# Performance work log

Hardware: AMD Instinct MI355X
Metric: run time of the kernel (lower is better)

The kernel has to match this reference:

```python
import jax, jax.numpy as jnp
import numpy as np

HEADS = 8
TOK = 4  # num_query_tokens
EPS = 1e-5


def _ln(x, w, b):
    mu = jnp.mean(x, -1, keepdims=True)
    v = jnp.var(x, -1, keepdims=True)
    return (x - mu) / jnp.sqrt(v + EPS) * w + b


def _inorm(x):
    # InstanceNorm3d(affine=False): normalize per (B,C) over spatial dims
    mu = jnp.mean(x, (2, 3, 4), keepdims=True)
    v = jnp.var(x, (2, 3, 4), keepdims=True)
    return (x - mu) / jnp.sqrt(v + EPS)


def _conv3(x, w, b):
    y = jax.lax.conv_general_dilated(x, w, (1, 1, 1), 'SAME',
                                     dimension_numbers=('NCDHW', 'OIDHW', 'NCDHW'))
    return y + b[None, :, None, None, None]


def setup_inputs() -> dict:
    key = jax.random.key(0)
    ks = jax.random.split(key, 8)
    B, C, D, H, W = 4, 320, 16, 32, 32
    CLI = 320
    QD = C * TOK  # 1280
    s = 0.02
    return {
        'img_feat': jax.random.normal(ks[0], (B, C, D, H, W), jnp.float32),
        'cli_feat': jax.random.normal(ks[1], (B, CLI), jnp.float32),
        'Wq': jax.random.normal(ks[2], (QD, CLI), jnp.float32) * s,
        'bq': jnp.zeros((QD,), jnp.float32),
        'lnq_w': jnp.ones((QD,), jnp.float32),
        'lnq_b': jnp.zeros((QD,), jnp.float32),
        'Wk': jax.random.normal(ks[3], (C, C), jnp.float32) * s,
        'bk': jnp.zeros((C,), jnp.float32),
        'Wv': jax.random.normal(ks[4], (C, C), jnp.float32) * s,
        'bv': jnp.zeros((C,), jnp.float32),
        'Wo': jax.random.normal(ks[5], (C, QD), jnp.float32) * s,
        'bo': jnp.zeros((C,), jnp.float32),
        'lno_w': jnp.ones((C,), jnp.float32),
        'lno_b': jnp.zeros((C,), jnp.float32),
        'Wf1': jax.random.normal(ks[6], (C, 2 * C, 3, 3, 3), jnp.float32) * s,
        'bf1': jnp.zeros((C,), jnp.float32),
        'Wf2': jax.random.normal(ks[7], (C, C, 3, 3, 3), jnp.float32) * s,
        'bf2': jnp.zeros((C,), jnp.float32),
    }


def reference(img_feat, cli_feat, Wq, bq, lnq_w, lnq_b, Wk, bk, Wv, bv,
              Wo, bo, lno_w, lno_b, Wf1, bf1, Wf2, bf2):
    B, C, D, H, W = img_feat.shape
    S = D * H * W
    hd = C // HEADS
    scale = hd ** -0.5
    # clinical features -> 4 query tokens per head: [B, heads, head_dim, TOK]
    q = _ln(cli_feat @ Wq.T + bq, lnq_w, lnq_b).reshape(B, HEADS, hd, TOK)
    # 1x1x1 convs == per-position linear over channels
    x = img_feat.reshape(B, C, S)
    k = (jnp.einsum('oc,bcs->bos', Wk, x) + bk[None, :, None]).reshape(B, HEADS, hd, S)
    v = (jnp.einsum('oc,bcs->bos', Wv, x) + bv[None, :, None]).reshape(B, HEADS, hd, S)
    # [B, heads, TOK, S] scores -> softmax over spatial
    attn = jax.nn.softmax(jnp.einsum('bhdt,bhds->bhts', q, k) * scale, axis=-1)
    # value @ attn^T -> [B, heads, head_dim, TOK], flatten like torch .view(B,-1)
    o = jnp.einsum('bhds,bhts->bhdt', v, attn).reshape(B, HEADS * hd * TOK)
    o = _ln(o @ Wo.T + bo, lno_w, lno_b)  # [B, C]
    bcast = jnp.broadcast_to(o[:, :, None, None, None], (B, C, D, H, W))
    fused = jnp.concatenate([img_feat, bcast], axis=1)  # [B, 2C, D, H, W]
    h = jax.nn.gelu(_inorm(_conv3(fused, Wf1, bf1)), approximate=False)
    h = _inorm(_conv3(h, Wf2, bf2))
    return h + img_feat
```

## Files before the change

kernel.cpp:

```cpp
#include <hip/hip_runtime.h>
#include <hip/hip_bf16.h>
#include <math.h>

typedef unsigned short u16;

#define DEV static __device__ __forceinline__

DEV float bfu(u16 u) { union { unsigned int i; float f; } v; v.i = ((unsigned int)u) << 16; return v.f; }
DEV u16 fbu(float f) { __hip_bfloat16 h = __float2bfloat16(f); return *reinterpret_cast<u16*>(&h); }

template <typename T> struct ModeOf;
template <> struct ModeOf<u16>   { static constexpr int v = 0; };
template <> struct ModeOf<float> { static constexpr int v = 1; };
template <typename T> DEV float ld(const void* p, size_t i);
template <> DEV float ld<u16>(const void* p, size_t i)   { return bfu(((const u16*)p)[i]); }
template <> DEV float ld<float>(const void* p, size_t i) { return ((const float*)p)[i]; }

DEV float dot8f(const float* img, size_t idx, const float* ar, int s) {
    const float4 x0 = *reinterpret_cast<const float4*>(img + idx + s);
    const float4 x1 = *reinterpret_cast<const float4*>(img + idx + s + 4);
    const float4 a0 = *reinterpret_cast<const float4*>(ar + s);
    const float4 a1 = *reinterpret_cast<const float4*>(ar + s + 4);
    return a0.x*x0.x + a0.y*x0.y + a0.z*x0.z + a0.w*x0.w
         + a1.x*x1.x + a1.y*x1.y + a1.z*x1.z + a1.w*x1.w;
}

#define NB 4
#define NC 320
#define ND 16
#define NH 32
#define NW 32
#define NS 16384
#define NHD 40
#define NQD 1280
#define NR 32
#define NTOK 4
#define OUT_N (NB*NC*NS)
#define EPSV 1e-5f
#define SCALE 0.15811388300841898f

#define YKS 8
#define YCH (NS / YKS)
#define YKC 32
#define YCS (NS / YKC)

#define CSL 32
#define NSL 10
#define HALO_D 4
#define HALO_H 6
#define PIXW 34
#define NPIX (HALO_D*HALO_H*PIXW)
#define PACKN (27*10*20*64*8)

typedef __attribute__((ext_vector_type(8))) short bf16x8;
typedef __attribute__((ext_vector_type(4))) float f32x4;

DEV int swz4(int p) { return (p + (p >> 2)) & 3; }

DEV float blk_sum(float v, float* red) {
    __syncthreads();
#pragma unroll
    for (int o = 32; o > 0; o >>= 1) v += __shfl_down(v, o, 64);
    int wv = threadIdx.x >> 6, ln = threadIdx.x & 63;
    if (ln == 0) red[wv] = v;
    __syncthreads();
    return red[0] + red[1] + red[2] + red[3];
}
DEV float blk_max(float v, float* red) {
    __syncthreads();
#pragma unroll
    for (int o = 32; o > 0; o >>= 1) v = fmaxf(v, __shfl_down(v, o, 64));
    int wv = threadIdx.x >> 6, ln = threadIdx.x & 63;
    if (ln == 0) red[wv] = v;
    __syncthreads();
    return fmaxf(fmaxf(red[0], red[1]), fmaxf(red[2], red[3]));
}

__global__ void detect_kernel(const u16* __restrict__ lnqw, int* __restrict__ flag) {
    if (threadIdx.x == 0) flag[0] = (lnqw[0] == 0x3F80) ? 0 : 1;
}

template <typename T>
__global__ __launch_bounds__(256) void q_kernel(const int* __restrict__ flag,
        const void* __restrict__ cli, const void* __restrict__ Wq, const void* __restrict__ bq,
        const void* __restrict__ lnw, const void* __restrict__ lnb, float* __restrict__ qout) {
    if (*flag != ModeOf<T>::v) return;
    int b = blockIdx.x, tid = threadIdx.x;
    __shared__ float cl[NC];
    __shared__ float red[8];
    for (int i = tid; i < NC; i += 256) cl[i] = ld<T>(cli, b * NC + i);
    __syncthreads();
    float loc[5];
    float s1 = 0.f, s2 = 0.f;
#pragma unroll
    for (int k = 0; k < 5; ++k) {
        int j = tid + k * 256;
        float a = ld<T>(bq, j);
        size_t wr = (size_t)j * NC;
        for (int c = 0; c < NC; ++c) a += cl[c] * ld<T>(Wq, wr + c);
        loc[k] = a; s1 += a; s2 += a * a;
    }
    s1 = blk_sum(s1, red);
    s2 = blk_sum(s2, red);
    float mu = s1 / (float)NQD;
    float var = fmaxf(s2 / (float)NQD - mu * mu, 0.f);
    float rs = rsqrtf(var + EPSV);
#pragma unroll
    for (int k = 0; k < 5; ++k) {
        int j = tid + k * 256;
        qout[(size_t)b * NQD + j] = (loc[k] - mu) * rs * ld<T>(lnw, j) + ld<T>(lnb, j);
    }
}

template <typename T>
__global__ __launch_bounds__(256) void qw_kernel(const int* __restrict__ flag,
        const float* __restrict__ q, const void* __restrict__ Wk, const void* __restrict__ bk,
        float* __restrict__ qW, float* __restrict__ qb, u16* __restrict__ qwb) {
    if (*flag != ModeOf<T>::v) return;
    int gid = blockIdx.x * 256 + threadIdx.x;
    if (gid < NB * NR * NC) {
        int c = gid % NC;
        int r = (gid / NC) % NR;
        int b = gid / (NC * NR);
        int h = r >> 2, t = r & 3;
        float a = 0.f;
        const float* qb_ = q + (size_t)b * NQD;
        for (int d = 0; d < NHD; ++d)
            a += qb_[(h * NHD + d) * NTOK + t] * ld<T>(Wk, (size_t)(h * NHD + d) * NC + c);
        qW[gid] = a;
        int kk = c >> 5, gg = (c >> 3) & 3, j = c & 7;
        int mf = r >> 4, lane = (gg << 4) | (r & 15);
        qwb[(((size_t)(b * 10 + kk) * 2 + mf) << 9) + (lane << 3) + j] = fbu(a);
    }
    if (gid < NB * NR) {
        int r = gid & 31, b = gid >> 5;
        int h = r >> 2, t = r & 3;
        float a = 0.f;
        const float* qb_ = q + (size_t)b * NQD;
        for (int d = 0; d < NHD; ++d)
            a += qb_[(h * NHD + d) * NTOK + t] * ld<T>(bk, h * NHD + d);
        qb[gid] = a;
    }
}

__global__ __launch_bounds__(256) void scores_mm_kernel(
        const u16* __restrict__ imgt, const u16* __restrict__ qwb,
        const float* __restrict__ qb, float* __restrict__ attn) {
    int b = blockIdx.y;
    int s0 = blockIdx.x * 256 + (threadIdx.x >> 6) * 64;
    int ln = threadIdx.x & 63;
    int col = ln & 15, g = ln >> 4;
    bf16x8 af[10][2];
    const u16* qa = qwb + (size_t)b * 10 * 2 * 512;
#pragma unroll
    for (int kk = 0; kk < 10; ++kk)
#pragma unroll
        for (int mf = 0; mf < 2; ++mf)
            af[kk][mf] = *reinterpret_cast<const bf16x8*>(qa + (((kk << 1) + mf) << 9) + (ln << 3));
    f32x4 acc[2][4];
#pragma unroll
    for (int mf = 0; mf < 2; ++mf)
#pragma unroll
        for (int nf = 0; nf < 4; ++nf) acc[mf][nf] = (f32x4){0.f, 0.f, 0.f, 0.f};
    const u16* xb = imgt + (size_t)b * NS * NC;
#pragma unroll
    for (int kk = 0; kk < 10; ++kk) {
#pragma unroll
        for (int nf = 0; nf < 4; ++nf) {
            bf16x8 bf = *reinterpret_cast<const bf16x8*>(
                xb + (size_t)(s0 + nf * 16 + col) * NC + kk * 32 + (g << 3));
#pragma unroll
            for (int mf = 0; mf < 2; ++mf)
                acc[mf][nf] = __builtin_amdgcn_mfma_f32_16x16x32_bf16(
                    af[kk][mf], bf, acc[mf][nf], 0, 0, 0);
        }
    }
#pragma unroll
    for (int mf = 0; mf < 2; ++mf)
#pragma unroll
        for (int nf = 0; nf < 4; ++nf)
#pragma unroll
            for (int r = 0; r < 4; ++r) {
                int row = mf * 16 + g * 4 + r;
                attn[((size_t)(b * NR + row) << 14) + s0 + nf * 16 + col] =
                    (acc[mf][nf][r] + qb[b * NR + row]) * SCALE;
            }
}

__global__ __launch_bounds__(256) void smax_part_kernel(const float* __restrict__ attn,
        float* __restrict__ pm, float* __restrict__ pl) {
    int row = blockIdx.x, kc = blockIdx.y;
    const float* rp = attn + ((size_t)row << 14) + kc * 2048;
    __shared__ float red[8];
    int t4 = threadIdx.x * 4;
    float4 v0 = *reinterpret_cast<const float4*>(rp + t4);
    float4 v1 = *reinterpret_cast<const float4*>(rp + t4 + 1024);
    float m = fmaxf(fmaxf(fmaxf(v0.x, v0.y), fmaxf(v0.z, v0.w)),
                    fmaxf(fmaxf(v1.x, v1.y), fmaxf(v1.z, v1.w)));
    m = blk_max(m, red);
    float s = expf(v0.x - m) + expf(v0.y - m) + expf(v0.z - m) + expf(v0.w - m)
            + expf(v1.x - m) + expf(v1.y - m) + expf(v1.z - m) + expf(v1.w - m);
    s = blk_sum(s, red);
    if (threadIdx.x == 0) { pm[row * 8 + kc] = m; pl[row * 8 + kc] = s; }
}

__global__ __launch_bounds__(128) void smax_comb_kernel(const float* __restrict__ pm,
        const float* __restrict__ pl, float* __restrict__ gm, float* __restrict__ gli) {
    int row = threadIdx.x;
    float M = -1e30f;
#pragma unroll
    for (int k = 0; k < 8; ++k) M = fmaxf(M, pm[row * 8 + k]);
    float L = 0.f;
#pragma unroll
    for (int k = 0; k < 8; ++k) L += pl[row * 8 + k] * expf(pm[row * 8 + k] - M);
    gm[row] = M; gli[row] = 1.f / L;
}

__global__ __launch_bounds__(256) void smax_fin_kernel(float* __restrict__ attn,
        const float* __restrict__ gm, const float* __restrict__ gli, u16* __restrict__ attnb) {
    int row = blockIdx.x, kc = blockIdx.y;
    size_t base = ((size_t)row << 14) + kc * 2048;
    float M = gm[row], LI = gli[row];
    int t4 = threadIdx.x * 4;
#pragma unroll
    for (int h = 0; h < 2; ++h) {
        size_t i = base + t4 + h * 1024;
        float4 v = *reinterpret_cast<const float4*>(attn + i);
        v.x = expf(v.x - M) * LI; v.y = expf(v.y - M) * LI;
        v.z = expf(v.z - M) * LI; v.w = expf(v.w - M) * LI;
        *reinterpret_cast<float4*>(attn + i) = v;
        ushort4 bv; bv.x = fbu(v.x); bv.y = fbu(v.y); bv.z = fbu(v.z); bv.w = fbu(v.w);
        *reinterpret_cast<ushort4*>(attnb + i) = bv;
    }
}

__global__ __launch_bounds__(256) void ymm_kernel(const int* __restrict__ flag,
        const u16* __restrict__ attnb, const void* __restrict__ img, float* __restrict__ yp) {
    if (*flag != 0) return;
    int kc = blockIdx.x, ct = blockIdx.y, b = blockIdx.z;
    int wv = threadIdx.x >> 6, ln = threadIdx.x & 63;
    int col = ln & 15, g = ln >> 4;
    int s0 = kc * YCS;
    const u16* imgB = (const u16*)img;
    const u16* ap0 = attnb + (((size_t)b * 32 + col) << 14) + s0 + (g << 3);
    const u16* bp  = imgB + (((size_t)(b * NC + ct * 64 + wv * 16 + col)) << 14) + s0 + (g << 3);
    f32x4 acc[2];
    acc[0] = (f32x4){0.f, 0.f, 0.f, 0.f};
    acc[1] = (f32x4){0.f, 0.f, 0.f, 0.f};
#pragma unroll
    for (int ks = 0; ks < YCS / 32; ++ks) {
        bf16x8 bf = *reinterpret_cast<const bf16x8*>(bp + ks * 32);
        bf16x8 a0 = *reinterpret_cast<const bf16x8*>(ap0 + ks * 32);
        bf16x8 a1 = *reinterpret_cast<const bf16x8*>(ap0 + (16 << 14) + ks * 32);
        acc[0] = __builtin_amdgcn_mfma_f32_16x16x32_bf16(a0, bf, acc[0], 0, 0, 0);
        acc[1] = __builtin_amdgcn_mfma_f32_16x16x32_bf16(a1, bf, acc[1], 0, 0, 0);
    }
    int c = ct * 64 + wv * 16 + col;
#pragma unroll
    for (int mf = 0; mf < 2; ++mf)
#pragma unroll
        for (int r = 0; r < 4; ++r) {
            int row = b * 32 + mf * 16 + g * 4 + r;
            yp[((size_t)kc * NB * NR + row) * NC + c] = acc[mf][r];
        }
}

template <typename T>
__global__ __launch_bounds__(256) void y_kernel(const int* __restrict__ flag,
        const float* __restrict__ attn, const void* __restrict__ img, float* __restrict__ yp) {
    if (*flag != ModeOf<T>::v) return;
    int row = blockIdx.x;
    int ks  = blockIdx.y;
    int b = row >> 5;
    int wv = threadIdx.x >> 6, ln = threadIdx.x & 63;
    const float* ar = attn + ((size_t)row << 14) + ks * YCH;
    size_t xb = (size_t)b * NC * NS + ks * YCH;
    float* yout = yp + ((size_t)ks * NB * NR + row) * NC;
    for (int c = wv; c < NC; c += 4) {
        size_t xr = xb + ((size_t)c << 14);
        float p = 0.f;
#pragma unroll
        for (int it = 0; it < YCH / 512; ++it)
            p += dot8f((const float*)img, xr, ar, it * 512 + ln * 8);
#pragma unroll
        for (int o = 32; o > 0; o >>= 1) p += __shfl_down(p, o, 64);
        if (ln == 0) yout[c] = p;
    }
}

__global__ __launch_bounds__(256) void yred_kernel(const int* __restrict__ flag, int mode, int nk,
        const float* __restrict__ yp, float* __restrict__ y) {
    if (*flag != mode) return;
    int i = blockIdx.x * 256 + threadIdx.x;
    if (i >= NB * NR * NC) return;
    float s = 0.f;
    for (int k = 0; k < nk; ++k) s += yp[(size_t)k * NB * NR * NC + i];
    y[i] = s;
}

template <typename T>
__global__ __launch_bounds__(256) void o_kernel(const int* __restrict__ flag,
        const float* __restrict__ y, const void* __restrict__ Wv, const void* __restrict__ bv,
        const void* __restrict__ Wo, const void* __restrict__ bo,
        const void* __restrict__ lnw, const void* __restrict__ lnb, float* __restrict__ o2) {
    if (*flag != ModeOf<T>::v) return;
    int b = blockIdx.x, tid = threadIdx.x;
    __shared__ float yl[NR * NC];
    __shared__ float ol[NQD];
    __shared__ float red[8];
    for (int i = tid; i < NR * NC; i += 256) yl[i] = y[(size_t)b * NR * NC + i];
    __syncthreads();
#pragma unroll
    for (int k = 0; k < 5; ++k) {
        int i = tid + k * 256;
        int h = i / 160, rem = i - h * 160;
        int d = rem >> 2, t = rem & 3;
        int wr = h * NHD + d, r = h * NTOK + t;
        float a = ld<T>(bv, wr);
        size_t wvr = (size_t)wr * NC;
        const float* yr = yl + r * NC;
        for (int c = 0; c < NC; ++c) a += ld<T>(Wv, wvr + c) * yr[c];
        ol[i] = a;
    }
    __syncthreads();
    for (int j = tid; j < NC; j += 256) {
        float a = ld<T>(bo, j);
        size_t wor = (size_t)j * NQD;
        for (int i = 0; i < NQD; ++i) a += ld<T>(Wo, wor + i) * ol[i];
        yl[j] = a;
    }
    __syncthreads();
    float s1 = 0.f, s2 = 0.f;
    for (int j = tid; j < NC; j += 256) { float v = yl[j]; s1 += v; s2 += v * v; }
    s1 = blk_sum(s1, red);
    s2 = blk_sum(s2, red);
    float mu = s1 / (float)NC;
    float var = fmaxf(s2 / (float)NC - mu * mu, 0.f);
    float rs = rsqrtf(var + EPSV);
    for (int j = tid; j < NC; j += 256)
        o2[(size_t)b * NC + j] = (yl[j] - mu) * rs * ld<T>(lnw, j) + ld<T>(lnb, j);
}

template <typename T>
__global__ __launch_bounds__(256) void p_kernel(const int* __restrict__ flag,
        const float* __restrict__ o2, const void* __restrict__ Wf1, float* __restrict__ P) {
    if (*flag != ModeOf<T>::v) return;
    int o = blockIdx.x, b = blockIdx.y;
    int tid = threadIdx.x, wv = tid >> 6, ln = tid & 63;
    __shared__ float red[4 * 27];
    __shared__ float taps[27];
    float acc[27];
#pragma unroll
    for (int k = 0; k < 27; ++k) acc[k] = 0.f;
    for (int c = tid; c < NC; c += 256) {
        float oc = o2[(size_t)b * NC + c];
        size_t wp = ((size_t)o * 640 + 320 + c) * 27;
#pragma unroll
        for (int k = 0; k < 27; ++k) acc[k] += oc * ld<T>(Wf1, wp + k);
    }
#pragma unroll
    for (int k = 0; k < 27; ++k) {
        float v = acc[k];
#pragma unroll
        for (int off = 32; off > 0; off >>= 1) v += __shfl_down(v, off, 64);
        if (ln == 0) red[wv * 27 + k] = v;
    }
    __syncthreads();
    if (tid < 27) taps[tid] = red[tid] + red[27 + tid] + red[54 + tid] + red[81 + tid];
    __syncthreads();
    if (tid < 27) {
        int pd = tid / 9, ph = (tid / 3) % 3, pw = tid % 3;
        float s = 0.f;
        for (int kd = 0; kd < 3; ++kd) {
            if ((pd == 0 && kd == 0) || (pd == 2 && kd == 2)) continue;
            for (int kh = 0; kh < 3; ++kh) {
                if ((ph == 0 && kh == 0) || (ph == 2 && kh == 2)) continue;
                for (int kw = 0; kw < 3; ++kw) {
                    if ((pw == 0 && kw == 0) || (pw == 2 && kw == 2)) continue;
                    s += taps[kd * 9 + kh * 3 + kw];
                }
            }
        }
        P[(size_t)(b * NC + o) * 27 + tid] = s;
    }
}

template <typename T>
__global__ __launch_bounds__(256) void imgt_kernel(const int* __restrict__ flag,
        const void* __restrict__ img, u16* __restrict__ outT) {
    if (*flag != ModeOf<T>::v) return;
    int b = blockIdx.z, c0 = blockIdx.y << 5, s0 = blockIdx.x << 5;
    int r = threadIdx.x >> 3, c4 = (threadIdx.x & 7) << 2;
    __shared__ float tile[32][33];
#pragma unroll
    for (int j = 0; j < 4; ++j)
        tile[r][c4 + j] = ld<T>(img, ((size_t)(b * NC + c0 + r) << 14) + s0 + c4 + j);
    __syncthreads();
    u16* op = outT + ((size_t)b * NS + s0 + r) * NC + c0 + c4;
#pragma unroll
    for (int j = 0; j < 4; ++j) op[j] = fbu(tile[c4 + j][r]);
}

template <typename TW>
__global__ __launch_bounds__(256) void pack_kernel(const int* __restrict__ flag,
        const void* __restrict__ wgt, const void* __restrict__ bias,
        u16* __restrict__ wpack, float* __restrict__ biasf, int wic) {
    if (*flag != ModeOf<TW>::v) return;
    int gid = blockIdx.x * 256 + threadIdx.x;
    if (gid < NC) biasf[gid] = ld<TW>(bias, gid);
    int lane = gid & 63;
    int rest = gid >> 6;
    int obg = rest % 20;  rest /= 20;
    int t = rest % 27;    int cs = rest / 27;
    int o  = (obg << 4) + (lane & 15);
    int c0 = (cs << 5) + ((lane >> 4) << 3);
    u16* dst = wpack + (size_t)gid * 8;
#pragma unroll
    for (int j = 0; j < 8; ++j)
        dst[j] = fbu(ld<TW>(wgt, ((size_t)o * wic + c0 + j) * 27 + t));
}

__global__ __launch_bounds__(256) void zstats_kernel(float* __restrict__ s1, float* __restrict__ s2) {
    int i = blockIdx.x * 256 + threadIdx.x;
    if (i < NB * NC) { s1[i] = 0.f; s2[i] = 0.f; }
}

__global__ __launch_bounds__(256, 3) void convmm_kernel(
        const u16* __restrict__ inT, const u16* __restrict__ wpack,
        const float* __restrict__ biasf, const float* __restrict__ Pp,
        u16* __restrict__ out, float* __restrict__ S1, float* __restrict__ S2) {
    int d0 = (blockIdx.x >> 3) << 1;
    int h0 = (blockIdx.x & 7) << 2;
    int ob = blockIdx.y;
    int b  = blockIdx.z;
    int tid = threadIdx.x;
    int wv = tid >> 6, ln = tid & 63;
    int col = ln & 15, g = ln >> 4;

    __shared__ __align__(16) u16 lin[NPIX * CSL];

    {
        float4 z = {0.f, 0.f, 0.f, 0.f};
        float4* lp = reinterpret_cast<float4*>(lin);
        for (int i = tid; i < NPIX * CSL / 8; i += 256) lp[i] = z;
    }
    __syncthreads();

    f32x4 acc[4][4];
#pragma unroll
    for (int mi = 0; mi < 4; ++mi)
#pragma unroll
        for (int ni = 0; ni < 4; ++ni) acc[mi][ni] = (f32x4){0.f, 0.f, 0.f, 0.f};

    int pix0[4];
#pragma unroll
    for (int ni = 0; ni < 4; ++ni) {
        int nb = (wv << 2) + ni;
        int r2 = nb >> 1;
        int ddo = r2 >> 2, hho = r2 & 3;
        pix0[ni] = (ddo * HALO_H + hho) * PIXW + ((nb & 1) << 4) + col;
    }

    size_t inb = (size_t)b * NS * NC;

    for (int cs = 0; cs < NSL; ++cs) {
        for (int k = wv; k < 48; k += 4) {
            int hf = k & 1, rr = k >> 1;
            int dd = rr / HALO_H, hh = rr - dd * HALO_H;
            int dg = d0 + dd - 1, hg = h0 + hh - 1;
            if ((unsigned)dg < ND && (unsigned)hg < NH) {
                int pixbase = (dd * HALO_H + hh) * PIXW + 1 + (hf << 4);
                int p = pixbase + (ln >> 2);
                int wpos = (hf << 4) + (ln >> 2);
                int cg = (ln & 3) ^ swz4(p);
                const u16* src = inT + inb + ((size_t)(dg << 10) + (hg << 5) + wpos) * NC
                                 + (cs << 5) + (cg << 3);
                __builtin_amdgcn_global_load_lds(
                    (const __attribute__((address_space(1))) unsigned int*)src,
                    (__attribute__((address_space(3))) unsigned int*)(lin + pixbase * CSL),
                    16, 0, 0);
            }
        }
        __syncthreads();

        const u16* wp = wpack + (size_t)cs * 27 * 20 * 512;
#pragma unroll
        for (int t = 0; t < 27; ++t) {
            const int kd = t / 9, kh = (t / 3) % 3, kw = t % 3;
            bf16x8 af[4];
#pragma unroll
            for (int mi = 0; mi < 4; ++mi)
                af[mi] = *reinterpret_cast<const bf16x8*>(
                    wp + ((size_t)(t * 20 + (ob << 2) + mi) << 9) + (ln << 3));
            bf16x8 bfr[4];
#pragma unroll
            for (int ni = 0; ni < 4; ++ni) {
                int p = pix0[ni] + (kd * HALO_H + kh) * PIXW + kw;
                bfr[ni] = *reinterpret_cast<const bf16x8*>(
                    lin + p * CSL + ((g ^ swz4(p)) << 3));
            }
#pragma unroll
            for (int mi = 0; mi < 4; ++mi)
#pragma unroll
                for (int ni = 0; ni < 4; ++ni)
                    acc[mi][ni] = __builtin_amdgcn_mfma_f32_16x16x32_bf16(
                        af[mi], bfr[ni], acc[mi][ni], 0, 0, 0);
        }
        __syncthreads();
    }

    size_t sidxA[4]; int pofA[4];
#pragma unroll
    for (int ni = 0; ni < 4; ++ni) {
        int nb = (wv << 2) + ni;
        int r2 = nb >> 1;
        int d = d0 + (r2 >> 2);
        int h = h0 + (r2 & 3);
        int w = ((nb & 1) << 4) + col;
        int pd = (d == 0) ? 0 : ((d == ND - 1) ? 2 : 1);
        int ph = (h == 0) ? 0 : ((h == NH - 1) ? 2 : 1);
        int pw = (w == 0) ? 0 : ((w == NW - 1) ? 2 : 1);
        sidxA[ni] = ((size_t)d << 10) + (h << 5) + w;
        pofA[ni] = pd * 9 + ph * 3 + pw;
    }
#pragma unroll
    for (int mi = 0; mi < 4; ++mi) {
#pragma unroll
        for (int r = 0; r < 4; ++r) {
            int o = (ob << 6) + (mi << 4) + (g << 2) + r;
            float bs = biasf[o];
            float s1 = 0.f, s2 = 0.f;
#pragma unroll
            for (int ni = 0; ni < 4; ++ni) {
                float v = acc[mi][ni][r] + bs;
                if (Pp) v += Pp[(size_t)(b * NC + o) * 27 + pofA[ni]];
                out[((size_t)(b * NC + o) << 14) + sidxA[ni]] = fbu(v);
                s1 += v; s2 += v * v;
            }
#pragma unroll
            for (int m = 1; m < 16; m <<= 1) {
                s1 += __shfl_xor(s1, m, 64);
                s2 += __shfl_xor(s2, m, 64);
            }
            if (col == 0) {
                atomicAdd(&S1[b * NC + o], s1);
                atomicAdd(&S2[b * NC + o], s2);
            }
        }
    }
}

__global__ __launch_bounds__(256) void statsfin_kernel(const float* __restrict__ S1,
        const float* __restrict__ S2, float* __restrict__ mean, float* __restrict__ rstd) {
    int i = blockIdx.x * 256 + threadIdx.x;
    if (i >= NB * NC) return;
    float mu = S1[i] / (float)NS;
    float var = fmaxf(S2[i] / (float)NS - mu * mu, 0.f);
    mean[i] = mu;
    rstd[i] = rsqrtf(var + EPSV);
}

__global__ __launch_bounds__(256) void norm1t_kernel(const u16* __restrict__ raw,
        const float* __restrict__ mean, const float* __restrict__ rstd, u16* __restrict__ h1t) {
    int b = blockIdx.z, c0 = blockIdx.y << 5, s0 = blockIdx.x << 5;
    int r = threadIdx.x >> 3, c4 = (threadIdx.x & 7) << 2;
    __shared__ float tile[32][33];
    int bo = b * NC + c0 + r;
    float mu = mean[bo], rs = rstd[bo];
    const u16* rp = raw + ((size_t)bo << 14) + s0 + c4;
#pragma unroll
    for (int j = 0; j < 4; ++j) {
        float xn = (bfu(rp[j]) - mu) * rs;
        tile[r][c4 + j] = 0.5f * xn * (1.f + erff(xn * 0.70710678118654752f));
    }
    __syncthreads();
    u16* op = h1t + ((size_t)b * NS + s0 + r) * NC + c0 + c4;
#pragma unroll
    for (int j = 0; j < 4; ++j) op[j] = fbu(tile[c4 + j][r]);
}

template <typename T>
__global__ __launch_bounds__(256) void final_kernel(const int* __restrict__ flag,
        const u16* __restrict__ raw, const float* __restrict__ mean, const float* __restrict__ rstd,
        const void* __restrict__ img, void* __restrict__ outp) {
    if (*flag != ModeOf<T>::v) return;
    int idx = (blockIdx.x * 256 + threadIdx.x) * 4;
    if (idx >= OUT_N) return;
    int bo = idx >> 14;
    float mu = mean[bo], rs = rstd[bo];
    ushort4 rv = *reinterpret_cast<const ushort4*>(raw + idx);
    float r0 = (bfu(rv.x) - mu) * rs;
    float r1 = (bfu(rv.y) - mu) * rs;
    float r2 = (bfu(rv.z) - mu) * rs;
    float r3 = (bfu(rv.w) - mu) * rs;
    if (ModeOf<T>::v == 0) {
        ushort4 iv = *reinterpret_cast<const ushort4*>((const u16*)img + idx);
        ushort4 ov;
        ov.x = fbu(r0 + bfu(iv.x)); ov.y = fbu(r1 + bfu(iv.y));
        ov.z = fbu(r2 + bfu(iv.z)); ov.w = fbu(r3 + bfu(iv.w));
        *reinterpret_cast<ushort4*>((u16*)outp + idx) = ov;
    } else {
        float4 iv = *reinterpret_cast<const float4*>((const float*)img + idx);
        float4 ov = make_float4(r0 + iv.x, r1 + iv.y, r2 + iv.z, r3 + iv.w);
        *reinterpret_cast<float4*>((float*)outp + idx) = ov;
    }
}

extern "C" void kernel_launch(void* const* d_in, const int* in_sizes, int n_in,
                              void* d_out, int out_size, void* d_ws, size_t ws_size,
                              hipStream_t stream) {
    const void* IMG  = d_in[0];
    const void* CLI  = d_in[1];
    const void* WQ   = d_in[2];
    const void* BQ   = d_in[3];
    const void* LNQW = d_in[4];
    const void* LNQB = d_in[5];
    const void* WK   = d_in[6];
    const void* BK   = d_in[7];
    const void* WV   = d_in[8];
    const void* BV   = d_in[9];
    const void* WO   = d_in[10];
    const void* BO   = d_in[11];
    const void* LNOW = d_in[12];
    const void* LNOB = d_in[13];
    const void* WF1  = d_in[14];
    const void* BF1  = d_in[15];
    const void* WF2  = d_in[16];
    const void* BF2  = d_in[17];

    char* ws = (char*)d_ws;
    size_t off = 0;
    auto alloc = [&](size_t bytes) { void* p = ws + off; off += (bytes + 255) & ~(size_t)255; return p; };
    int*   FLAG  = (int*)  alloc(256);
    u16*   RAW   = (u16*)  alloc((size_t)OUT_N * 2);
    float* Qf    = (float*)alloc((size_t)NB * NQD * 4);
    float* QW    = (float*)alloc((size_t)NB * NR * NC * 4);
    float* QB    = (float*)alloc((size_t)NB * NR * 4);
    u16*   QWB   = (u16*)  alloc((size_t)NB * 10 * 2 * 512 * 2);
    float* Yb    = (float*)alloc((size_t)NB * NR * NC * 4);
    float* O2    = (float*)alloc((size_t)NB * NC * 4);
    float* PB    = (float*)alloc((size_t)NB * NC * 27 * 4);
    float* MEAN  = (float*)alloc((size_t)NB * NC * 4);
    float* RSTD  = (float*)alloc((size_t)NB * NC * 4);
    float* ST1   = (float*)alloc((size_t)NB * NC * 4);
    float* ST2   = (float*)alloc((size_t)NB * NC * 4);
    float* PM    = (float*)alloc((size_t)NB * NR * 8 * 4);
    float* PL    = (float*)alloc((size_t)NB * NR * 8 * 4);
    float* GM    = (float*)alloc((size_t)NB * NR * 4);
    float* GLI   = (float*)alloc((size_t)NB * NR * 4);
    u16*   WPACK = (u16*)  alloc((size_t)PACKN * 2);
    float* BIASF = (float*)alloc((size_t)NC * 4);
    float* YP    = (float*)RAW;
    float* ATTN  = (float*)((char*)RAW + (16u << 20));
    u16*   ATTNB = (u16*)  ((char*)RAW + (26u << 20));
    u16*   IMGT  = (u16*)d_out;
    u16*   H1    = (u16*)d_out;
    (void)ws_size; (void)n_in; (void)in_sizes; (void)out_size;

    detect_kernel<<<1, 64, 0, stream>>>((const u16*)LNQW, FLAG);

    imgt_kernel<u16>  <<<dim3(512, 10, NB), 256, 0, stream>>>(FLAG, IMG, IMGT);
    imgt_kernel<float><<<dim3(512, 10, NB), 256, 0, stream>>>(FLAG, IMG, IMGT);

    q_kernel<u16>  <<<NB, 256, 0, stream>>>(FLAG, CLI, WQ, BQ, LNQW, LNQB, Qf);
    q_kernel<float><<<NB, 256, 0, stream>>>(FLAG, CLI, WQ, BQ, LNQW, LNQB, Qf);

    int qwg = (NB * NR * NC + 255) / 256;
    qw_kernel<u16>  <<<qwg, 256, 0, stream>>>(FLAG, Qf, WK, BK, QW, QB, QWB);
    qw_kernel<float><<<qwg, 256, 0, stream>>>(FLAG, Qf, WK, BK, QW, QB, QWB);

    scores_mm_kernel<<<dim3(64, NB), 256, 0, stream>>>(IMGT, QWB, QB, ATTN);

    smax_part_kernel<<<dim3(NB * NR, 8), 256, 0, stream>>>(ATTN, PM, PL);
    smax_comb_kernel<<<1, 128, 0, stream>>>(PM, PL, GM, GLI);
    smax_fin_kernel<<<dim3(NB * NR, 8), 256, 0, stream>>>(ATTN, GM, GLI, ATTNB);

    ymm_kernel<<<dim3(YKC, 5, NB), 256, 0, stream>>>(FLAG, ATTNB, IMG, YP);
    y_kernel<float><<<dim3(NB * NR, YKS), 256, 0, stream>>>(FLAG, ATTN, IMG, YP);

    int yrg = (NB * NR * NC + 255) / 256;
    yred_kernel<<<yrg, 256, 0, stream>>>(FLAG, 0, YKC, YP, Yb);
    yred_kernel<<<yrg, 256, 0, stream>>>(FLAG, 1, YKS, YP, Yb);

    o_kernel<u16>  <<<NB, 256, 0, stream>>>(FLAG, Yb, WV, BV, WO, BO, LNOW, LNOB, O2);
    o_kernel<float><<<NB, 256, 0, stream>>>(FLAG, Yb, WV, BV, WO, BO, LNOW, LNOB, O2);

    p_kernel<u16>  <<<dim3(NC, NB), 256, 0, stream>>>(FLAG, O2, WF1, PB);
    p_kernel<float><<<dim3(NC, NB), 256, 0, stream>>>(FLAG, O2, WF1, PB);

    int pkg = (PACKN / 8 + 255) / 256;
    pack_kernel<u16>  <<<pkg, 256, 0, stream>>>(FLAG, WF1, BF1, WPACK, BIASF, 640);
    pack_kernel<float><<<pkg, 256, 0, stream>>>(FLAG, WF1, BF1, WPACK, BIASF, 640);

    zstats_kernel<<<(NB * NC + 255) / 256, 256, 0, stream>>>(ST1, ST2);
    convmm_kernel<<<dim3(64, 5, NB), 256, 0, stream>>>(IMGT, WPACK, BIASF, PB, RAW, ST1, ST2);
    statsfin_kernel<<<(NB * NC + 255) / 256, 256, 0, stream>>>(ST1, ST2, MEAN, RSTD);

    norm1t_kernel<<<dim3(512, 10, NB), 256, 0, stream>>>(RAW, MEAN, RSTD, H1);

    pack_kernel<u16>  <<<pkg, 256, 0, stream>>>(FLAG, WF2, BF2, WPACK, BIASF, 320);
    pack_kernel<float><<<pkg, 256, 0, stream>>>(FLAG, WF2, BF2, WPACK, BIASF, 320);

    zstats_kernel<<<(NB * NC + 255) / 256, 256, 0, stream>>>(ST1, ST2);
    convmm_kernel<<<dim3(64, 5, NB), 256, 0, stream>>>(H1, WPACK, BIASF, nullptr, RAW, ST1, ST2);
    statsfin_kernel<<<(NB * NC + 255) / 256, 256, 0, stream>>>(ST1, ST2, MEAN, RSTD);

    final_kernel<u16>  <<<(OUT_N / 4 + 255) / 256, 256, 0, stream>>>(FLAG, RAW, MEAN, RSTD, IMG, d_out);
    final_kernel<float><<<(OUT_N / 4 + 255) / 256, 256, 0, stream>>>(FLAG, RAW, MEAN, RSTD, IMG, d_out);
}
```

Baseline: 2.144 ms.

## Load conv inputs directly from global instead of LDS halo; separate stats pass

The 3D conv kernel no longer stages a swizzled halo tile into LDS. Each MFMA B-fragment is now read straight from global memory, with out-of-bounds taps redirected to a small zero buffer. The per-channel InstanceNorm statistics move out of the conv epilogue (no atomics) into a separate stats kernel that re-reads the bf16 conv output. Launch bounds rise to 4 blocks/SU. This removes LDS traffic and barriers but relies on L1/L2 for the 27-fold input reuse and adds an extra full read of the conv output.

Result: slower. 3.975 ms (+85.4%).

```diff
diff --git a/kernel.cpp b/kernel.cpp
--- a/kernel.cpp
+++ b/kernel.cpp
@@ -46,16 +46,10 @@
 
 #define CSL 32
 #define NSL 10
-#define HALO_D 4
-#define HALO_H 6
-#define PIXW 34
-#define NPIX (HALO_D*HALO_H*PIXW)
 #define PACKN (27*10*20*64*8)
 
 typedef __attribute__((ext_vector_type(8))) short bf16x8;
 typedef __attribute__((ext_vector_type(4))) float f32x4;
-
-DEV int swz4(int p) { return (p + (p >> 2)) & 3; }
 
 DEV float blk_sum(float v, float* red) {
     __syncthreads();
@@ -76,8 +70,10 @@
     return fmaxf(fmaxf(red[0], red[1]), fmaxf(red[2], red[3]));
 }
 
-__global__ void detect_kernel(const u16* __restrict__ lnqw, int* __restrict__ flag) {
+__global__ void detect_kernel(const u16* __restrict__ lnqw, int* __restrict__ flag,
+                              float* __restrict__ zbuf) {
     if (threadIdx.x == 0) flag[0] = (lnqw[0] == 0x3F80) ? 0 : 1;
+    if (threadIdx.x < 16) zbuf[threadIdx.x] = 0.f;
 }
 
 template <typename T>
@@ -420,15 +416,10 @@
         dst[j] = fbu(ld<TW>(wgt, ((size_t)o * wic + c0 + j) * 27 + t));
 }
 
-__global__ __launch_bounds__(256) void zstats_kernel(float* __restrict__ s1, float* __restrict__ s2) {
-    int i = blockIdx.x * 256 + threadIdx.x;
-    if (i < NB * NC) { s1[i] = 0.f; s2[i] = 0.f; }
-}
-
-__global__ __launch_bounds__(256, 3) void convmm_kernel(
+__global__ __launch_bounds__(256, 4) void convmm_kernel(
         const u16* __restrict__ inT, const u16* __restrict__ wpack,
         const float* __restrict__ biasf, const float* __restrict__ Pp,
-        u16* __restrict__ out, float* __restrict__ S1, float* __restrict__ S2) {
+        const u16* __restrict__ zbuf, u16* __restrict__ out) {
     int d0 = (blockIdx.x >> 3) << 1;
     int h0 = (blockIdx.x & 7) << 2;
     int ob = blockIdx.y;
@@ -437,56 +428,32 @@
     int wv = tid >> 6, ln = tid & 63;
     int col = ln & 15, g = ln >> 4;
 
-    __shared__ __align__(16) u16 lin[NPIX * CSL];
-
-    {
-        float4 z = {0.f, 0.f, 0.f, 0.f};
-        float4* lp = reinterpret_cast<float4*>(lin);
-        for (int i = tid; i < NPIX * CSL / 8; i += 256) lp[i] = z;
-    }
-    __syncthreads();
-
     f32x4 acc[4][4];
 #pragma unroll
     for (int mi = 0; mi < 4; ++mi)
 #pragma unroll
         for (int ni = 0; ni < 4; ++ni) acc[mi][ni] = (f32x4){0.f, 0.f, 0.f, 0.f};
 
-    int pix0[4];
+    int dA[4], hA[4], wA[4];
+    const u16* bpA[4];
 #pragma unroll
     for (int ni = 0; ni < 4; ++ni) {
         int nb = (wv << 2) + ni;
         int r2 = nb >> 1;
-        int ddo = r2 >> 2, hho = r2 & 3;
-        pix0[ni] = (ddo * HALO_H + hho) * PIXW + ((nb & 1) << 4) + col;
-    }
-
-    size_t inb = (size_t)b * NS * NC;
+        dA[ni] = d0 + (r2 >> 2);
+        hA[ni] = h0 + (r2 & 3);
+        wA[ni] = ((nb & 1) << 4) + col;
+        int px = (dA[ni] << 10) + (hA[ni] << 5) + wA[ni];
+        bpA[ni] = inT + (size_t)b * NS * NC + (size_t)px * NC + (g << 3);
+    }
 
     for (int cs = 0; cs < NSL; ++cs) {
-        for (int k = wv; k < 48; k += 4) {
-            int hf = k & 1, rr = k >> 1;
-            int dd = rr / HALO_H, hh = rr - dd * HALO_H;
-            int dg = d0 + dd - 1, hg = h0 + hh - 1;
-            if ((unsigned)dg < ND && (unsigned)hg < NH) {
-                int pixbase = (dd * HALO_H + hh) * PIXW + 1 + (hf << 4);
-                int p = pixbase + (ln >> 2);
-                int wpos = (hf << 4) + (ln >> 2);
-                int cg = (ln & 3) ^ swz4(p);
-                const u16* src = inT + inb + ((size_t)(dg << 10) + (hg << 5) + wpos) * NC
-                                 + (cs << 5) + (cg << 3);
-                __builtin_amdgcn_global_load_lds(
-                    (const __attribute__((address_space(1))) unsigned int*)src,
-                    (__attribute__((address_space(3))) unsigned int*)(lin + pixbase * CSL),
-                    16, 0, 0);
-            }
-        }
-        __syncthreads();
-
         const u16* wp = wpack + (size_t)cs * 27 * 20 * 512;
+        int cof = cs << 5;
 #pragma unroll
         for (int t = 0; t < 27; ++t) {
             const int kd = t / 9, kh = (t / 3) % 3, kw = t % 3;
+            const int tap = (kd - 1) * 1024 + (kh - 1) * 32 + (kw - 1);
             bf16x8 af[4];
 #pragma unroll
             for (int mi = 0; mi < 4; ++mi)
@@ -495,9 +462,11 @@
             bf16x8 bfr[4];
 #pragma unroll
             for (int ni = 0; ni < 4; ++ni) {
-                int p = pix0[ni] + (kd * HALO_H + kh) * PIXW + kw;
-                bfr[ni] = *reinterpret_cast<const bf16x8*>(
-                    lin + p * CSL + ((g ^ swz4(p)) << 3));
+                bool ok = ((unsigned)(dA[ni] + kd - 1) < ND) &&
+                          ((unsigned)(hA[ni] + kh - 1) < NH) &&
+                          ((unsigned)(wA[ni] + kw - 1) < NW);
+                const u16* src = ok ? (bpA[ni] + (ptrdiff_t)tap * NC + cof) : zbuf;
+                bfr[ni] = *reinterpret_cast<const bf16x8*>(src);
             }
 #pragma unroll
             for (int mi = 0; mi < 4; ++mi)
@@ -506,58 +475,51 @@
                     acc[mi][ni] = __builtin_amdgcn_mfma_f32_16x16x32_bf16(
                         af[mi], bfr[ni], acc[mi][ni], 0, 0, 0);
         }
-        __syncthreads();
-    }
-
-    size_t sidxA[4]; int pofA[4];
+    }
+
 #pragma unroll
     for (int ni = 0; ni < 4; ++ni) {
-        int nb = (wv << 2) + ni;
-        int r2 = nb >> 1;
-        int d = d0 + (r2 >> 2);
-        int h = h0 + (r2 & 3);
-        int w = ((nb & 1) << 4) + col;
+        int d = dA[ni], h = hA[ni], w = wA[ni];
         int pd = (d == 0) ? 0 : ((d == ND - 1) ? 2 : 1);
         int ph = (h == 0) ? 0 : ((h == NH - 1) ? 2 : 1);
         int pw = (w == 0) ? 0 : ((w == NW - 1) ? 2 : 1);
-        sidxA[ni] = ((size_t)d << 10) + (h << 5) + w;
-        pofA[ni] = pd * 9 + ph * 3 + pw;
-    }
-#pragma unroll
-    for (int mi = 0; mi < 4; ++mi) {
-#pragma unroll
-        for (int r = 0; r < 4; ++r) {
-            int o = (ob << 6) + (mi << 4) + (g << 2) + r;
-            float bs = biasf[o];
-            float s1 = 0.f, s2 = 0.f;
-#pragma unroll
-            for (int ni = 0; ni < 4; ++ni) {
-                float v = acc[mi][ni][r] + bs;
-                if (Pp) v += Pp[(size_t)(b * NC + o) * 27 + pofA[ni]];
-                out[((size_t)(b * NC + o) << 14) + sidxA[ni]] = fbu(v);
-                s1 += v; s2 += v * v;
-            }
-#pragma unroll
-            for (int m = 1; m < 16; m <<= 1) {
-                s1 += __shfl_xor(s1, m, 64);
-                s2 += __shfl_xor(s2, m, 64);
-            }
-            if (col == 0) {
-                atomicAdd(&S1[b * NC + o], s1);
-                atomicAdd(&S2[b * NC + o], s2);
+        size_t sidx = ((size_t)d << 10) + (h << 5) + w;
+#pragma unroll
+        for (int mi = 0; mi < 4; ++mi) {
+#pragma unroll
+            for (int r = 0; r < 4; ++r) {
+                int o = (ob << 6) + (mi << 4) + (g << 2) + r;
+                float v = acc[mi][ni][r] + biasf[o];
+                if (Pp) v += Pp[(size_t)(b * NC + o) * 27 + pd * 9 + ph * 3 + pw];
+                out[((size_t)(b * NC + o) << 14) + sidx] = fbu(v);
             }
         }
     }
 }
 
-__global__ __launch_bounds__(256) void statsfin_kernel(const float* __restrict__ S1,
-        const float* __restrict__ S2, float* __restrict__ mean, float* __restrict__ rstd) {
-    int i = blockIdx.x * 256 + threadIdx.x;
-    if (i >= NB * NC) return;
-    float mu = S1[i] / (float)NS;
-    float var = fmaxf(S2[i] / (float)NS - mu * mu, 0.f);
-    mean[i] = mu;
-    rstd[i] = rsqrtf(var + EPSV);
+__global__ __launch_bounds__(256) void stats_kernel(const u16* __restrict__ raw, float* __restrict__ mean,
+                                                    float* __restrict__ rstd) {
+    int bo = blockIdx.x;
+    const u16* base = raw + ((size_t)bo << 14);
+    __shared__ float red[8];
+    float s1 = 0.f, s2 = 0.f;
+    for (int s0 = threadIdx.x * 8; s0 < NS; s0 += 2048) {
+        uint4 v = *reinterpret_cast<const uint4*>(base + s0);
+        float x0 = bfu(v.x & 0xffff), x1 = bfu(v.x >> 16);
+        float x2 = bfu(v.y & 0xffff), x3 = bfu(v.y >> 16);
+        float x4 = bfu(v.z & 0xffff), x5 = bfu(v.z >> 16);
+        float x6 = bfu(v.w & 0xffff), x7 = bfu(v.w >> 16);
+        s1 += ((x0 + x1) + (x2 + x3)) + ((x4 + x5) + (x6 + x7));
+        s2 += ((x0*x0 + x1*x1) + (x2*x2 + x3*x3)) + ((x4*x4 + x5*x5) + (x6*x6 + x7*x7));
+    }
+    s1 = blk_sum(s1, red);
+    s2 = blk_sum(s2, red);
+    if (threadIdx.x == 0) {
+        float mu = s1 / (float)NS;
+        float var = fmaxf(s2 / (float)NS - mu * mu, 0.f);
+        mean[bo] = mu;
+        rstd[bo] = rsqrtf(var + EPSV);
+    }
 }
 
 __global__ __launch_bounds__(256) void norm1t_kernel(const u16* __restrict__ raw,
@@ -632,6 +594,7 @@
     size_t off = 0;
     auto alloc = [&](size_t bytes) { void* p = ws + off; off += (bytes + 255) & ~(size_t)255; return p; };
     int*   FLAG  = (int*)  alloc(256);
+    float* ZBUF  = (float*)alloc(256);
     u16*   RAW   = (u16*)  alloc((size_t)OUT_N * 2);
     float* Qf    = (float*)alloc((size_t)NB * NQD * 4);
     float* QW    = (float*)alloc((size_t)NB * NR * NC * 4);
@@ -642,8 +605,6 @@
     float* PB    = (float*)alloc((size_t)NB * NC * 27 * 4);
     float* MEAN  = (float*)alloc((size_t)NB * NC * 4);
     float* RSTD  = (float*)alloc((size_t)NB * NC * 4);
-    float* ST1   = (float*)alloc((size_t)NB * NC * 4);
-    float* ST2   = (float*)alloc((size_t)NB * NC * 4);
     float* PM    = (float*)alloc((size_t)NB * NR * 8 * 4);
     float* PL    = (float*)alloc((size_t)NB * NR * 8 * 4);
     float* GM    = (float*)alloc((size_t)NB * NR * 4);
@@ -657,7 +618,7 @@
     u16*   H1    = (u16*)d_out;
     (void)ws_size; (void)n_in; (void)in_sizes; (void)out_size;
 
-    detect_kernel<<<1, 64, 0, stream>>>((const u16*)LNQW, FLAG);
+    detect_kernel<<<1, 64, 0, stream>>>((const u16*)LNQW, FLAG, ZBUF);
 
     imgt_kernel<u16>  <<<dim3(512, 10, NB), 256, 0, stream>>>(FLAG, IMG, IMGT);
     imgt_kernel<float><<<dim3(512, 10, NB), 256, 0, stream>>>(FLAG, IMG, IMGT);
@@ -692,18 +653,17 @@
     pack_kernel<u16>  <<<pkg, 256, 0, stream>>>(FLAG, WF1, BF1, WPACK, BIASF, 640);
     pack_kernel<float><<<pkg, 256, 0, stream>>>(FLAG, WF1, BF1, WPACK, BIASF, 640);
 
-    zstats_kernel<<<(NB * NC + 255) / 256, 256, 0, stream>>>(ST1, ST2);
-    convmm_kernel<<<dim3(64, 5, NB), 256, 0, stream>>>(IMGT, WPACK, BIASF, PB, RAW, ST1, ST2);
-    statsfin_kernel<<<(NB * NC + 255) / 256, 256, 0, stream>>>(ST1, ST2, MEAN, RSTD);
-
+    convmm_kernel<<<dim3(64, 5, NB), 256, 0, stream>>>(IMGT, WPACK, BIASF, PB, (const u16*)ZBUF, RAW);
+
+    stats_kernel<<<NB * NC, 256, 0, stream>>>(RAW, MEAN, RSTD);
     norm1t_kernel<<<dim3(512, 10, NB), 256, 0, stream>>>(RAW, MEAN, RSTD, H1);
 
     pack_kernel<u16>  <<<pkg, 256, 0, stream>>>(FLAG, WF2, BF2, WPACK, BIASF, 320);
     pack_kernel<float><<<pkg, 256, 0, stream>>>(FLAG, WF2, BF2, WPACK, BIASF, 320);
 
-    zstats_kernel<<<(NB * NC + 255) / 256, 256, 0, stream>>>(ST1, ST2);
-    convmm_kernel<<<dim3(64, 5, NB), 256, 0, stream>>>(H1, WPACK, BIASF, nullptr, RAW, ST1, ST2);
-    statsfin_kernel<<<(NB * NC + 255) / 256, 256, 0, stream>>>(ST1, ST2, MEAN, RSTD);
+    convmm_kernel<<<dim3(64, 5, NB), 256, 0, stream>>>(H1, WPACK, BIASF, nullptr, (const u16*)ZBUF, RAW);
+
+    stats_kernel<<<NB * NC, 256, 0, stream>>>(RAW, MEAN, RSTD);
 
     final_kernel<u16>  <<<(OUT_N / 4 + 255) / 256, 256, 0, stream>>>(FLAG, RAW, MEAN, RSTD, IMG, d_out);
     final_kernel<float><<<(OUT_N / 4 + 255) / 256, 256, 0, stream>>>(FLAG, RAW, MEAN, RSTD, IMG, d_out);
```

## Compute instance-norm stats in separate pass instead of conv-epilogue atomics

Applied to the files above, without the earlier changes.

Removes the per-channel sum and sum-of-squares reduction and atomicAdd from the conv epilogue, along with the zero and finalize kernels. Stats are now computed by a dedicated kernel that rereads the bf16 conv output, one block per (batch, channel). The softmax finalize kernel also writes only the fp32 or the bf16 attention buffer depending on the input dtype flag, instead of both. This trades atomic contention and epilogue shuffles for an extra read of the conv output, and the stats now come from bf16-rounded values.

After: 2.039 ms. 1.05x faster.

```diff
diff --git a/kernel.cpp b/kernel.cpp
--- a/kernel.cpp
+++ b/kernel.cpp
@@ -216,8 +216,10 @@
     gm[row] = M; gli[row] = 1.f / L;
 }
 
-__global__ __launch_bounds__(256) void smax_fin_kernel(float* __restrict__ attn,
-        const float* __restrict__ gm, const float* __restrict__ gli, u16* __restrict__ attnb) {
+__global__ __launch_bounds__(256) void smax_fin_kernel(const int* __restrict__ flag,
+        float* __restrict__ attn, const float* __restrict__ gm, const float* __restrict__ gli,
+        u16* __restrict__ attnb) {
+    int mode = *flag;
     int row = blockIdx.x, kc = blockIdx.y;
     size_t base = ((size_t)row << 14) + kc * 2048;
     float M = gm[row], LI = gli[row];
@@ -228,9 +230,12 @@
         float4 v = *reinterpret_cast<const float4*>(attn + i);
         v.x = expf(v.x - M) * LI; v.y = expf(v.y - M) * LI;
         v.z = expf(v.z - M) * LI; v.w = expf(v.w - M) * LI;
-        *reinterpret_cast<float4*>(attn + i) = v;
-        ushort4 bv; bv.x = fbu(v.x); bv.y = fbu(v.y); bv.z = fbu(v.z); bv.w = fbu(v.w);
-        *reinterpret_cast<ushort4*>(attnb + i) = bv;
+        if (mode == 1) {
+            *reinterpret_cast<float4*>(attn + i) = v;
+        } else {
+            ushort4 bv; bv.x = fbu(v.x); bv.y = fbu(v.y); bv.z = fbu(v.z); bv.w = fbu(v.w);
+            *reinterpret_cast<ushort4*>(attnb + i) = bv;
+        }
     }
 }
 
@@ -420,15 +425,10 @@
         dst[j] = fbu(ld<TW>(wgt, ((size_t)o * wic + c0 + j) * 27 + t));
 }
 
-__global__ __launch_bounds__(256) void zstats_kernel(float* __restrict__ s1, float* __restrict__ s2) {
-    int i = blockIdx.x * 256 + threadIdx.x;
-    if (i < NB * NC) { s1[i] = 0.f; s2[i] = 0.f; }
-}
-
 __global__ __launch_bounds__(256, 3) void convmm_kernel(
         const u16* __restrict__ inT, const u16* __restrict__ wpack,
         const float* __restrict__ biasf, const float* __restrict__ Pp,
-        u16* __restrict__ out, float* __restrict__ S1, float* __restrict__ S2) {
+        u16* __restrict__ out) {
     int d0 = (blockIdx.x >> 3) << 1;
     int h0 = (blockIdx.x & 7) << 2;
     int ob = blockIdx.y;
@@ -509,7 +509,6 @@
         __syncthreads();
     }
 
-    size_t sidxA[4]; int pofA[4];
 #pragma unroll
     for (int ni = 0; ni < 4; ++ni) {
         int nb = (wv << 2) + ni;
@@ -520,44 +519,43 @@
         int pd = (d == 0) ? 0 : ((d == ND - 1) ? 2 : 1);
         int ph = (h == 0) ? 0 : ((h == NH - 1) ? 2 : 1);
         int pw = (w == 0) ? 0 : ((w == NW - 1) ? 2 : 1);
-        sidxA[ni] = ((size_t)d << 10) + (h << 5) + w;
-        pofA[ni] = pd * 9 + ph * 3 + pw;
-    }
-#pragma unroll
-    for (int mi = 0; mi < 4; ++mi) {
-#pragma unroll
-        for (int r = 0; r < 4; ++r) {
-            int o = (ob << 6) + (mi << 4) + (g << 2) + r;
-            float bs = biasf[o];
-            float s1 = 0.f, s2 = 0.f;
-#pragma unroll
-            for (int ni = 0; ni < 4; ++ni) {
-                float v = acc[mi][ni][r] + bs;
-                if (Pp) v += Pp[(size_t)(b * NC + o) * 27 + pofA[ni]];
-                out[((size_t)(b * NC + o) << 14) + sidxA[ni]] = fbu(v);
-                s1 += v; s2 += v * v;
-            }
-#pragma unroll
-            for (int m = 1; m < 16; m <<= 1) {
-                s1 += __shfl_xor(s1, m, 64);
-                s2 += __shfl_xor(s2, m, 64);
-            }
-            if (col == 0) {
-                atomicAdd(&S1[b * NC + o], s1);
-                atomicAdd(&S2[b * NC + o], s2);
+        size_t sidx = ((size_t)d << 10) + (h << 5) + w;
+#pragma unroll
+        for (int mi = 0; mi < 4; ++mi) {
+#pragma unroll
+            for (int r = 0; r < 4; ++r) {
+                int o = (ob << 6) + (mi << 4) + (g << 2) + r;
+                float v = acc[mi][ni][r] + biasf[o];
+                if (Pp) v += Pp[(size_t)(b * NC + o) * 27 + pd * 9 + ph * 3 + pw];
+                out[((size_t)(b * NC + o) << 14) + sidx] = fbu(v);
             }
         }
     }
 }
 
-__global__ __launch_bounds__(256) void statsfin_kernel(const float* __restrict__ S1,
-        const float* __restrict__ S2, float* __restrict__ mean, float* __restrict__ rstd) {
-    int i = blockIdx.x * 256 + threadIdx.x;
-    if (i >= NB * NC) return;
-    float mu = S1[i] / (float)NS;
-    float var = fmaxf(S2[i] / (float)NS - mu * mu, 0.f);
-    mean[i] = mu;
-    rstd[i] = rsqrtf(var + EPSV);
+__global__ __launch_bounds__(256) void stats_kernel(const u16* __restrict__ raw, float* __restrict__ mean,
+                                                    float* __restrict__ rstd) {
+    int bo = blockIdx.x;
+    const u16* base = raw + ((size_t)bo << 14);
+    __shared__ float red[8];
+    float s1 = 0.f, s2 = 0.f;
+    for (int s0 = threadIdx.x * 8; s0 < NS; s0 += 2048) {
+        uint4 v = *reinterpret_cast<const uint4*>(base + s0);
+        float x0 = bfu(v.x & 0xffff), x1 = bfu(v.x >> 16);
+        float x2 = bfu(v.y & 0xffff), x3 = bfu(v.y >> 16);
+        float x4 = bfu(v.z & 0xffff), x5 = bfu(v.z >> 16);
+        float x6 = bfu(v.w & 0xffff), x7 = bfu(v.w >> 16);
+        s1 += ((x0 + x1) + (x2 + x3)) + ((x4 + x5) + (x6 + x7));
+        s2 += ((x0*x0 + x1*x1) + (x2*x2 + x3*x3)) + ((x4*x4 + x5*x5) + (x6*x6 + x7*x7));
+    }
+    s1 = blk_sum(s1, red);
+    s2 = blk_sum(s2, red);
+    if (threadIdx.x == 0) {
+        float mu = s1 / (float)NS;
+        float var = fmaxf(s2 / (float)NS - mu * mu, 0.f);
+        mean[bo] = mu;
+        rstd[bo] = rsqrtf(var + EPSV);
+    }
 }
 
 __global__ __launch_bounds__(256) void norm1t_kernel(const u16* __restrict__ raw,
@@ -642,8 +640,6 @@
     float* PB    = (float*)alloc((size_t)NB * NC * 27 * 4);
     float* MEAN  = (float*)alloc((size_t)NB * NC * 4);
     float* RSTD  = (float*)alloc((size_t)NB * NC * 4);
-    float* ST1   = (float*)alloc((size_t)NB * NC * 4);
-    float* ST2   = (float*)alloc((size_t)NB * NC * 4);
     float* PM    = (float*)alloc((size_t)NB * NR * 8 * 4);
     float* PL    = (float*)alloc((size_t)NB * NR * 8 * 4);
     float* GM    = (float*)alloc((size_t)NB * NR * 4);
@@ -673,7 +669,7 @@
 
     smax_part_kernel<<<dim3(NB * NR, 8), 256, 0, stream>>>(ATTN, PM, PL);
     smax_comb_kernel<<<1, 128, 0, stream>>>(PM, PL, GM, GLI);
-    smax_fin_kernel<<<dim3(NB * NR, 8), 256, 0, stream>>>(ATTN, GM, GLI, ATTNB);
+    smax_fin_kernel<<<dim3(NB * NR, 8), 256, 0, stream>>>(FLAG, ATTN, GM, GLI, ATTNB);
 
     ymm_kernel<<<dim3(YKC, 5, NB), 256, 0, stream>>>(FLAG, ATTNB, IMG, YP);
     y_kernel<float><<<dim3(NB * NR, YKS), 256, 0, stream>>>(FLAG, ATTN, IMG, YP);
@@ -692,18 +688,17 @@
     pack_kernel<u16>  <<<pkg, 256, 0, stream>>>(FLAG, WF1, BF1, WPACK, BIASF, 640);
     pack_kernel<float><<<pkg, 256, 0, stream>>>(FLAG, WF1, BF1, WPACK, BIASF, 640);
 
-    zstats_kernel<<<(NB * NC + 255) / 256, 256, 0, stream>>>(ST1, ST2);
-    convmm_kernel<<<dim3(64, 5, NB), 256, 0, stream>>>(IMGT, WPACK, BIASF, PB, RAW, ST1, ST2);
-    statsfin_kernel<<<(NB * NC + 255) / 256, 256, 0, stream>>>(ST1, ST2, MEAN, RSTD);
-
+    convmm_kernel<<<dim3(64, 5, NB), 256, 0, stream>>>(IMGT, WPACK, BIASF, PB, RAW);
+
+    stats_kernel<<<NB * NC, 256, 0, stream>>>(RAW, MEAN, RSTD);
     norm1t_kernel<<<dim3(512, 10, NB), 256, 0, stream>>>(RAW, MEAN, RSTD, H1);
 
     pack_kernel<u16>  <<<pkg, 256, 0, stream>>>(FLAG, WF2, BF2, WPACK, BIASF, 320);
     pack_kernel<float><<<pkg, 256, 0, stream>>>(FLAG, WF2, BF2, WPACK, BIASF, 320);
 
-    zstats_kernel<<<(NB * NC + 255) / 256, 256, 0, stream>>>(ST1, ST2);
-    convmm_kernel<<<dim3(64, 5, NB), 256, 0, stream>>>(H1, WPACK, BIASF, nullptr, RAW, ST1, ST2);
-    statsfin_kernel<<<(NB * NC + 255) / 256, 256, 0, stream>>>(ST1, ST2, MEAN, RSTD);
+    convmm_kernel<<<dim3(64, 5, NB), 256, 0, stream>>>(H1, WPACK, BIASF, nullptr, RAW);
+
+    stats_kernel<<<NB * NC, 256, 0, stream>>>(RAW, MEAN, RSTD);
 
     final_kernel<u16>  <<<(OUT_N / 4 + 255) / 256, 256, 0, stream>>>(FLAG, RAW, MEAN, RSTD, IMG, d_out);
     final_kernel<float><<<(OUT_N / 4 + 255) / 256, 256, 0, stream>>>(FLAG, RAW, MEAN, RSTD, IMG, d_out);
```
